# Kernel tuning notes

Measured on AMD Instinct MI355X. Metric: run time of the kernel, lower is better.

The kernel has to match this reference:

```python
import jax, jax.numpy as jnp
import numpy as np
import math

B, S, D, H, DF, L = 8, 1024, 1024, 16, 4096, 2
DK = D // H

def cosine_pe(seq_len, d_model):
    pos = jnp.arange(seq_len, dtype=jnp.float32)[:, None]
    div = jnp.exp(jnp.arange(0, d_model, 2, dtype=jnp.float32) * (-math.log(10000.0) / d_model))
    ang = pos * div[None, :]  # [S, D/2]
    # interleave sin (even cols) and cos (odd cols)
    return jnp.stack([jnp.sin(ang), jnp.cos(ang)], axis=-1).reshape(seq_len, d_model)

def layernorm(x, g, b, eps=1e-5):
    m = jnp.mean(x, axis=-1, keepdims=True)
    v = jnp.mean((x - m) ** 2, axis=-1, keepdims=True)
    return (x - m) / jnp.sqrt(v + eps) * g + b

def setup_inputs() -> dict:
    key = jax.random.key(0)
    ks = jax.random.split(key, 8)
    w = 0.03  # ~xavier scale for d_model=1024
    return {
        "q_embed_data": jax.random.normal(ks[0], (B, S, D), dtype=jnp.float32),
        "qa_embed_data": jax.random.normal(ks[1], (B, S, D), dtype=jnp.float32),
        "Wk": jax.random.normal(ks[2], (L, D, D), dtype=jnp.float32) * w,
        "bk": jnp.zeros((L, D), jnp.float32),
        "Wv": jax.random.normal(ks[3], (L, D, D), dtype=jnp.float32) * w,
        "bv": jnp.zeros((L, D), jnp.float32),
        "Wo": jax.random.normal(ks[4], (L, D, D), dtype=jnp.float32) * w,
        "bo": jnp.zeros((L, D), jnp.float32),
        "ln1_g": jnp.ones((L, D), jnp.float32),
        "ln1_b": jnp.zeros((L, D), jnp.float32),
        "W1": jax.random.normal(ks[5], (L, DF, D), dtype=jnp.float32) * w,
        "b1": jnp.zeros((L, DF), jnp.float32),
        "W2": jax.random.normal(ks[6], (L, D, DF), dtype=jnp.float32) * w,
        "b2": jnp.zeros((L, D), jnp.float32),
        "ln2_g": jnp.ones((L, D), jnp.float32),
        "ln2_b": jnp.zeros((L, D), jnp.float32),
    }

def reference(q_embed_data, qa_embed_data, Wk, bk, Wv, bv, Wo, bo, ln1_g, ln1_b, W1, b1, W2, b2, ln2_g, ln2_b):
    b, s, d = q_embed_data.shape
    pe = cosine_pe(s, d)
    x = q_embed_data + pe[None]   # query/key stream, updated per block
    y = qa_embed_data + pe[None]  # value stream, fixed across blocks
    idx = jnp.arange(s)
    allow = idx[None, :] < idx[:, None]  # strict causal: only past (j < i)
    n_blocks = Wk.shape[0]
    for l in range(n_blocks):
        # kq_same=True: q and k share k_linear
        q = (x @ Wk[l].T + bk[l]).reshape(b, s, H, DK).transpose(0, 2, 1, 3)
        k = q  # same input and same projection
        v = (y @ Wv[l].T + bv[l]).reshape(b, s, H, DK).transpose(0, 2, 1, 3)
        scores = jnp.einsum('bhid,bhjd->bhij', q, k) / math.sqrt(DK)
        scores = jnp.where(allow[None, None], scores, jnp.float32(-1e32))
        p = jax.nn.softmax(scores, axis=-1)
        p = p.at[:, :, 0, :].set(0.0)  # zero_pad first query row
        attn = jnp.einsum('bhij,bhjd->bhid', p, v).transpose(0, 2, 1, 3).reshape(b, s, d)
        attn = attn @ Wo[l].T + bo[l]
        x = layernorm(x + attn, ln1_g[l], ln1_b[l])
        ff = jax.nn.relu(x @ W1[l].T + b1[l]) @ W2[l].T + b2[l]
        x = layernorm(x + ff, ln2_g[l], ln2_b[l])
    return x
```

## Files before the change

kernel.cpp:

```cpp
#include <hip/hip_runtime.h>

using bf16   = __bf16;
using bf16x4 = __attribute__((ext_vector_type(4))) __bf16;
using bf16x8 = __attribute__((ext_vector_type(8))) __bf16;
using f32x4  = __attribute__((ext_vector_type(4))) float;

#define GLDS16(g, l)                                                            \
  __builtin_amdgcn_global_load_lds(                                             \
      (__attribute__((address_space(1))) void*)(g),                             \
      (__attribute__((address_space(3))) void*)(l), 16, 0, 0)

#define MFMA16(a, b, c) __builtin_amdgcn_mfma_f32_16x16x32_bf16(a, b, c, 0, 0, 0)

__device__ __forceinline__ int SW(int r, int s) {
  return r * 64 + (((s ^ (r & 7) ^ ((r >> 3) & 7)) & 7) << 3);
}

__device__ __forceinline__ float b2f(unsigned short u) {
  return (float)__builtin_bit_cast(bf16, u);
}

__device__ __forceinline__ bf16x8 scale8th(bf16x8 v) {
  bf16x8 r;
#pragma unroll
  for (int i = 0; i < 8; ++i) r[i] = (bf16)((float)v[i] * 0.125f);
  return r;
}

__global__ __launch_bounds__(256)
void init_pe(const float4* __restrict__ qd, const float4* __restrict__ qa,
             ushort4* __restrict__ xbf, ushort4* __restrict__ ybf) {
  const int n4 = 8 * 1024 * 1024 / 4;
  for (int i = blockIdx.x * 256 + threadIdx.x; i < n4; i += gridDim.x * 256) {
    int d4 = (i & 255) * 4;
    int ss = (i >> 8) & 1023;
    const float c = -0.0089944730195177f;
    float a0 = (float)ss * __expf((float)d4 * c);
    float a1 = (float)ss * __expf((float)(d4 + 2) * c);
    float p0 = sinf(a0), p1 = cosf(a0), p2 = sinf(a1), p3 = cosf(a1);
    float4 q4 = qd[i], y4 = qa[i];
    ushort4 xb, yb;
    xb.x = __builtin_bit_cast(unsigned short, (bf16)(q4.x + p0));
    xb.y = __builtin_bit_cast(unsigned short, (bf16)(q4.y + p1));
    xb.z = __builtin_bit_cast(unsigned short, (bf16)(q4.z + p2));
    xb.w = __builtin_bit_cast(unsigned short, (bf16)(q4.w + p3));
    yb.x = __builtin_bit_cast(unsigned short, (bf16)(y4.x + p0));
    yb.y = __builtin_bit_cast(unsigned short, (bf16)(y4.y + p1));
    yb.z = __builtin_bit_cast(unsigned short, (bf16)(y4.z + p2));
    yb.w = __builtin_bit_cast(unsigned short, (bf16)(y4.w + p3));
    xbf[i] = xb; ybf[i] = yb;
  }
}

__global__ __launch_bounds__(256)
void cvt5(const float4* __restrict__ s0, const float4* __restrict__ s1,
          const float4* __restrict__ s2, const float4* __restrict__ s3,
          const float4* __restrict__ s4,
          ushort4* __restrict__ dDD, ushort4* __restrict__ dDF,
          int n4dd, int n4df) {
  const int z = blockIdx.z;
  const float4* s = (z == 0) ? s0 : (z == 1) ? s1 : (z == 2) ? s2 : (z == 3) ? s3 : s4;
  ushort4* dd = (z < 3) ? dDD + (size_t)z * n4dd : dDF + (size_t)(z - 3) * n4df;
  const int n4 = (z < 3) ? n4dd : n4df;
  for (int i = blockIdx.x * 256 + threadIdx.x; i < n4; i += gridDim.x * 256) {
    float4 v = s[i];
    ushort4 o;
    o.x = __builtin_bit_cast(unsigned short, (bf16)v.x);
    o.y = __builtin_bit_cast(unsigned short, (bf16)v.y);
    o.z = __builtin_bit_cast(unsigned short, (bf16)v.z);
    o.w = __builtin_bit_cast(unsigned short, (bf16)v.w);
    dd[i] = o;
  }
}

template <int EPI, int MODE>
__global__ __launch_bounds__(256, 4)
void gemm_s(const bf16* __restrict__ A0, const bf16* __restrict__ W0,
            const float* __restrict__ b0, void* __restrict__ C0,
            const bf16* __restrict__ A1, const bf16* __restrict__ W1,
            const float* __restrict__ b1, void* __restrict__ C1,
            const int N, const int K) {
  __shared__ bf16 L[2][128 * 64];

  const int tid = threadIdx.x;
  const int wave = tid >> 6, lane = tid & 63;
  const int wm = wave >> 1, wn = wave & 1;
  const int cl = lane & 15, hk = lane >> 4;

  const int gx = gridDim.x;
  int flat = blockIdx.y * gx + blockIdx.x;
  flat = (flat & 7) * ((gx * gridDim.y) >> 3) + (flat >> 3);
  const int bcol = flat % gx, brow = flat / gx;
  const int z = (MODE == 0) ? 0 : blockIdx.z;

  const bf16* A = (MODE == 1 && z) ? A1 : A0;
  const bf16* W = (MODE == 1 && z) ? W1 : W0;
  const float* bias = (MODE == 1 && z) ? b1 : b0;
  void* C = (MODE == 1 && z) ? C1 : C0;

  const bf16* Ablk = A + (size_t)brow * 128 * K;
  const bf16* Wblk = W + (size_t)bcol * 128 * K;

  const int strow8 = lane >> 3;
  const int sl8 = (lane & 7) ^ (lane >> 3);

#define STAGE(kt)                                                               \
  do {                                                                          \
    _Pragma("unroll") for (int i_ = 0; i_ < 4; ++i_) {                          \
      int r0_ = i_ * 32 + wave * 8;                                             \
      GLDS16(Ablk + (size_t)(r0_ + strow8) * K + (size_t)(kt) * 64 + sl8 * 8,   \
             &L[0][r0_ * 64]);                                                  \
      GLDS16(Wblk + (size_t)(r0_ + strow8) * K + (size_t)(kt) * 64 + sl8 * 8,   \
             &L[1][r0_ * 64]);                                                  \
    }                                                                           \
  } while (0)

#define RD(reg, r_, kk_) \
  (*(const bf16x8*)&L[reg][(r_) * 64 + ((((kk_) * 4 + hk) ^ (cl & 7)) * 8)])

  f32x4 acc[4][4] = {};
  const int NT = K >> 6;

  for (int t = 0; t < NT; ++t) {
    STAGE(t);
    __syncthreads();
#pragma unroll
    for (int kk = 0; kk < 2; ++kk) {
      bf16x8 a4[4], b4[4];
#pragma unroll
      for (int m = 0; m < 4; ++m) a4[m] = RD(0, wm * 64 + m * 16 + cl, kk);
#pragma unroll
      for (int n = 0; n < 4; ++n) b4[n] = RD(1, wn * 64 + n * 16 + cl, kk);
      __builtin_amdgcn_s_setprio(1);
#pragma unroll
      for (int m = 0; m < 4; ++m)
#pragma unroll
        for (int n = 0; n < 4; ++n)
          acc[m][n] = MFMA16(a4[m], b4[n], acc[m][n]);
      __builtin_amdgcn_s_setprio(0);
    }
    __syncthreads();
  }
#undef STAGE
#undef RD

  float bv[4];
#pragma unroll
  for (int n = 0; n < 4; ++n)
    bv[n] = bias[bcol * 128 + wn * 64 + n * 16 + cl];

  const int crow0 = brow * 128 + wm * 64;
  const int ccol0 = bcol * 128 + wn * 64;
  char* esmem = (char*)(&L[0][0]) + wave * 4608;

  if (MODE == 1 && z == 1) {
    bf16* ep = (bf16*)esmem;
    const int h_ = ccol0 >> 6;
#pragma unroll
    for (int mp = 0; mp < 2; ++mp) {
#pragma unroll
      for (int mb = 0; mb < 2; ++mb) {
        int m = mp * 2 + mb;
#pragma unroll
        for (int n = 0; n < 4; ++n) {
          bf16x4 w4;
#pragma unroll
          for (int j = 0; j < 4; ++j) w4[j] = (bf16)(acc[m][n][j] + bv[n]);
          *(bf16x4*)&ep[(n * 16 + cl) * 36 + mb * 16 + hk * 4] = w4;
        }
      }
      asm volatile("s_waitcnt lgkmcnt(0)" ::: "memory");
      __builtin_amdgcn_sched_barrier(0);
      {
        const int t0 = crow0 + mp * 32;
        const int b_ = t0 >> 10, s_ = t0 & 1023;
        bf16* dst = (bf16*)C + ((size_t)(b_ * 16 + h_) * 64 + lane) * 1024 + s_;
        const bf16* src = &ep[lane * 36];
#pragma unroll
        for (int i = 0; i < 4; ++i)
          *(bf16x8*)&dst[i * 8] = *(const bf16x8*)&src[i * 8];
      }
      asm volatile("s_waitcnt lgkmcnt(0)" ::: "memory");
      __builtin_amdgcn_sched_barrier(0);
    }
  } else {
#pragma unroll
    for (int m = 0; m < 4; ++m) {
      bf16* ep = (bf16*)esmem;
#pragma unroll
      for (int n = 0; n < 4; ++n)
#pragma unroll
        for (int j = 0; j < 4; ++j) {
          float val = acc[m][n][j] + bv[n];
          if (EPI == 1) val = fmaxf(val, 0.f);
          ep[(hk * 4 + j) * 64 + n * 16 + cl] = (bf16)val;
        }
      asm volatile("s_waitcnt lgkmcnt(0)" ::: "memory");
      __builtin_amdgcn_sched_barrier(0);
#pragma unroll
      for (int i = 0; i < 2; ++i) {
        bf16x8 vv = ((const bf16x8*)ep)[lane + i * 64];
        const int row = crow0 + m * 16 + 8 * i + (lane >> 3);
        *(bf16x8*)((bf16*)C + (size_t)row * N + ccol0 + (lane & 7) * 8) = vv;
      }
      asm volatile("s_waitcnt lgkmcnt(0)" ::: "memory");
      __builtin_amdgcn_sched_barrier(0);
    }
  }
}

#define SOFTMAX_PV(sc_, diag_, mreg, lreg, oacc)                                 \
  do {                                                                           \
    if (diag_) {                                                                 \
      _Pragma("unroll") for (int c = 0; c < 4; ++c)                              \
        _Pragma("unroll") for (int j = 0; j < 4; ++j)                            \
          if (c * 16 + hk * 4 + j >= wave * 16 + cl) sc_[c][j] = -1e30f;         \
    }                                                                            \
    float rl_[4];                                                                \
    _Pragma("unroll") for (int c = 0; c < 4; ++c)                                \
      rl_[c] = fmaxf(fmaxf(sc_[c][0], sc_[c][1]), fmaxf(sc_[c][2], sc_[c][3]));  \
    float rloc_ = fmaxf(fmaxf(rl_[0], rl_[1]), fmaxf(rl_[2], rl_[3]));           \
    if (!__all(rloc_ <= mreg)) {                                                 \
      float rmx_ = fmaxf(rloc_, __shfl_xor(rloc_, 16));                          \
      rmx_ = fmaxf(rmx_, __shfl_xor(rmx_, 32));                                  \
      float mn_ = fmaxf(mreg, rmx_);                                             \
      float sca_ = __expf(mreg - mn_);                                           \
      mreg = mn_;                                                                \
      lreg *= sca_;                                                              \
      float scr_[4];                                                             \
      _Pragma("unroll") for (int j = 0; j < 4; ++j)                              \
        scr_[j] = __shfl(sca_, hk * 4 + j);                                      \
      _Pragma("unroll") for (int c = 0; c < 4; ++c)                              \
        _Pragma("unroll") for (int j = 0; j < 4; ++j) oacc[c][j] *= scr_[j];     \
    }                                                                            \
    float ps_ = 0.f;                                                             \
    if (diag_) {                                                                 \
      _Pragma("unroll") for (int c = 0; c < 4; ++c) {                            \
        bf16x4 pk_;                                                              \
        _Pragma("unroll") for (int j = 0; j < 4; ++j) {                          \
          float e_ = (sc_[c][j] < -1e29f) ? 0.f : __expf(sc_[c][j] - mreg);      \
          ps_ += e_;                                                             \
          pk_[j] = (bf16)e_;                                                     \
        }                                                                        \
        *(bf16x4*)&Pw[SW(cl, c * 2 + (hk >> 1)) + (hk & 1) * 4] = pk_;           \
      }                                                                          \
    } else {                                                                     \
      _Pragma("unroll") for (int c = 0; c < 4; ++c) {                            \
        bf16x4 pk_;                                                              \
        _Pragma("unroll") for (int j = 0; j < 4; ++j) {                          \
          float e_ = __expf(sc_[c][j] - mreg);                                   \
          ps_ += e_;                                                             \
          pk_[j] = (bf16)e_;                                                     \
        }                                                                        \
        *(bf16x4*)&Pw[SW(cl, c * 2 + (hk >> 1)) + (hk & 1) * 4] = pk_;           \
      }                                                                          \
    }                                                                            \
    lreg += ps_;                  \
    const bf16x8 pa0_ = *(const bf16x8*)&Pw[SW(cl, hk)];                         \
    const bf16x8 pa1_ = *(const bf16x8*)&Pw[SW(cl, 4 + hk)];                     \
    __builtin_amdgcn_s_setprio(1);                                               \
    _Pragma("unroll") for (int c = 0; c < 4; ++c) {                              \
      const bf16x8 vf0_ = *(const bf16x8*)&Vb[SW(c * 16 + cl, hk)];              \
      const bf16x8 vf1_ = *(const bf16x8*)&Vb[SW(c * 16 + cl, 4 + hk)];          \
      oacc[c] = MFMA16(pa0_, vf0_, oacc[c]);                                     \
      oacc[c] = MFMA16(pa1_, vf1_, oacc[c]);                                     \
    }                                                                            \
    __builtin_amdgcn_s_setprio(0);                                               \
  } while (0)

__global__ __launch_bounds__(256, 2)
void attn_kernel(const bf16* __restrict__ q, const bf16* __restrict__ vT,
                 bf16* __restrict__ out) {
  const int S = 1024, D = 1024;
  const int f = blockIdx.y * 8 + blockIdx.x;
  const int g = f >> 3, xcd = f & 7;
  const int qa = g >> 4;
  const int bh = xcd * 16 + (g & 15);
  const int qb = 15 - qa;
  const int b = bh >> 4, h = bh & 15;
  const int tid = threadIdx.x, wave = tid >> 6, lane = tid & 63;

  __shared__ bf16 Ks[2][4096];
  __shared__ bf16 Vt[2][4096];
  __shared__ bf16 Ps[4][1024];

  const bf16* qp = q + (size_t)b * S * D + h * 64;
  const bf16* vp = vT + (size_t)(b * 16 + h) * 64 * 1024;

  const int cl = lane & 15;
  const int hk = lane >> 4;
  const int r0 = hk * 4;
  const int k8 = hk * 8;

  const int ksrow = lane >> 3;
  const int ksslot = (lane & 7) ^ (lane >> 3);

  const int rA = qa * 64 + wave * 16 + cl;
  const int rB = qb * 64 + wave * 16 + cl;
  const bf16x8 qA0 = scale8th(*(const bf16x8*)(qp + (size_t)rA * D + k8));
  const bf16x8 qA1 = scale8th(*(const bf16x8*)(qp + (size_t)rA * D + 32 + k8));
  const bf16x8 qB0 = scale8th(*(const bf16x8*)(qp + (size_t)rB * D + k8));
  const bf16x8 qB1 = scale8th(*(const bf16x8*)(qp + (size_t)rB * D + 32 + k8));

  f32x4 oA[4] = {}, oB[4] = {};
  float mA_ = -1e30f, lA_ = 0.f, mB_ = -1e30f, lB_ = 0.f;

  bf16* Pw = Ps[wave];
  int buf = 0;

#define STAGE_KV(dst_ks, dst_vt, jt_)                                            \
  do {                                                                           \
    _Pragma("unroll") for (int j = 0; j < 2; ++j) {                              \
      int ch = wave * 2 + j;                                                     \
      GLDS16(qp + (size_t)((jt_) * 64 + ch * 8 + ksrow) * D +                    \
                 ((ksslot ^ (ch & 7)) * 8),                                      \
             (dst_ks) + ch * 512);                                               \
      GLDS16(vp + (size_t)(ch * 8 + ksrow) * 1024 + (jt_) * 64 +                 \
                 ((ksslot ^ (ch & 7)) * 8),                                      \
             (dst_vt) + ch * 512);                                               \
    }                                                                            \
  } while (0)

  STAGE_KV(&Ks[0][0], &Vt[0][0], 0);
  __syncthreads();

  for (int jt = 0; jt <= qb; ++jt) {
    const int nxt = buf ^ 1;
    if (jt < qb) STAGE_KV(&Ks[nxt][0], &Vt[nxt][0], jt + 1);

    {
      const bf16* Kb = Ks[buf];
      const bf16* Vb = Vt[buf];
      const bool doA = (jt <= qa);
      const bool diagB = (jt == qb), diagA = (jt == qa);

      f32x4 scB[4], scA[4];
      __builtin_amdgcn_s_setprio(1);
#pragma unroll
      for (int c = 0; c < 4; ++c) {
        int r_ = c * 16 + cl;
        const bf16x8 kf0 = *(const bf16x8*)&Kb[SW(r_, hk)];
        const bf16x8 kf1 = *(const bf16x8*)&Kb[SW(r_, 4 + hk)];
        f32x4 zB = {};
        zB = MFMA16(kf0, qB0, zB);
        zB = MFMA16(kf1, qB1, zB);
        scB[c] = zB;
        if (doA) {
          f32x4 zA = {};
          zA = MFMA16(kf0, qA0, zA);
          zA = MFMA16(kf1, qA1, zA);
          scA[c] = zA;
        }
      }
      __builtin_amdgcn_s_setprio(0);

      SOFTMAX_PV(scB, diagB, mB_, lB_, oB);
      if (doA) SOFTMAX_PV(scA, diagA, mA_, lA_, oA);
    }
    __syncthreads();
    buf = nxt;
  }
#undef STAGE_KV

  lA_ += __shfl_xor(lA_, 16);
  lA_ += __shfl_xor(lA_, 32);
  lB_ += __shfl_xor(lB_, 16);
  lB_ += __shfl_xor(lB_, 32);

  bf16* ob = out + (size_t)b * S * D + h * 64;
  const float invA = (lA_ > 0.f) ? 1.f / lA_ : 0.f;
  const float invB = (lB_ > 0.f) ? 1.f / lB_ : 0.f;
#pragma unroll
  for (int j = 0; j < 4; ++j) {
    const float iA = __shfl(invA, hk * 4 + j);
    const float iB = __shfl(invB, hk * 4 + j);
    {
      int row = qa * 64 + wave * 16 + r0 + j;
#pragma unroll
      for (int c = 0; c < 4; ++c)
        ob[(size_t)row * D + c * 16 + cl] = (bf16)(oA[c][j] * iA);
    }
    {
      int row = qb * 64 + wave * 16 + r0 + j;
#pragma unroll
      for (int c = 0; c < 4; ++c)
        ob[(size_t)row * D + c * 16 + cl] = (bf16)(oB[c][j] * iB);
    }
  }
}

__global__ __launch_bounds__(256)
void add_ln(const ushort4* __restrict__ xin, const ushort4* __restrict__ y1b,
            const float* __restrict__ g, const float* __restrict__ bt,
            ushort4* __restrict__ xbf, float4* __restrict__ xout) {
  const int row = blockIdx.x;
  const int tid = threadIdx.x;
  const int wave = tid >> 6, lane = tid & 63;
  const size_t base4 = (size_t)row * 256 + tid;
  ushort4 a4 = xin[base4];
  ushort4 c4 = y1b[base4];
  float v0 = b2f(a4.x) + b2f(c4.x), v1 = b2f(a4.y) + b2f(c4.y);
  float v2 = b2f(a4.z) + b2f(c4.z), v3 = b2f(a4.w) + b2f(c4.w);

  float s = v0 + v1 + v2 + v3;
#pragma unroll
  for (int off = 32; off; off >>= 1) s += __shfl_xor(s, off);
  __shared__ float red1[4], red2[4];
  if (lane == 0) red1[wave] = s;
  __syncthreads();
  float mean = (red1[0] + red1[1] + red1[2] + red1[3]) * (1.f / 1024.f);

  float d0 = v0 - mean, d1 = v1 - mean, d2 = v2 - mean, d3 = v3 - mean;
  float vs = d0 * d0 + d1 * d1 + d2 * d2 + d3 * d3;
#pragma unroll
  for (int off = 32; off; off >>= 1) vs += __shfl_xor(vs, off);
  if (lane == 0) red2[wave] = vs;
  __syncthreads();
  float var = (red2[0] + red2[1] + red2[2] + red2[3]) * (1.f / 1024.f);
  float rstd = rsqrtf(var + 1e-5f);

  const int col = tid * 4;
  float4 gg = *(const float4*)(g + col);
  float4 bb = *(const float4*)(bt + col);
  float o0 = d0 * rstd * gg.x + bb.x;
  float o1 = d1 * rstd * gg.y + bb.y;
  float o2 = d2 * rstd * gg.z + bb.z;
  float o3 = d3 * rstd * gg.w + bb.w;
  if (xout) {
    float4 oo; oo.x = o0; oo.y = o1; oo.z = o2; oo.w = o3;
    xout[base4] = oo;
  } else {
    ushort4 ob;
    ob.x = __builtin_bit_cast(unsigned short, (bf16)o0);
    ob.y = __builtin_bit_cast(unsigned short, (bf16)o1);
    ob.z = __builtin_bit_cast(unsigned short, (bf16)o2);
    ob.w = __builtin_bit_cast(unsigned short, (bf16)o3);
    xbf[base4] = ob;
  }
}

extern "C" void kernel_launch(void* const* d_in, const int* in_sizes, int n_in,
                              void* d_out, int out_size, void* d_ws, size_t ws_size,
                              hipStream_t stream) {
  const float* qd  = (const float*)d_in[0];
  const float* qa  = (const float*)d_in[1];
  const float* Wk  = (const float*)d_in[2];
  const float* bk  = (const float*)d_in[3];
  const float* Wv  = (const float*)d_in[4];
  const float* bv  = (const float*)d_in[5];
  const float* Wo  = (const float*)d_in[6];
  const float* bo  = (const float*)d_in[7];
  const float* l1g = (const float*)d_in[8];
  const float* l1b = (const float*)d_in[9];
  const float* W1  = (const float*)d_in[10];
  const float* b1  = (const float*)d_in[11];
  const float* W2  = (const float*)d_in[12];
  const float* b2  = (const float*)d_in[13];
  const float* l2g = (const float*)d_in[14];
  const float* l2b = (const float*)d_in[15];

  const size_t DD = 1024 * 1024, DFD = 4096 * 1024, T = 8192;
  bf16* wkb = (bf16*)d_ws;
  bf16* wvb = wkb + 2 * DD;
  bf16* wob = wvb + 2 * DD;
  bf16* w1b = wob + 2 * DD;
  bf16* w2b = w1b + 2 * DFD;
  bf16* regA = w2b + 2 * DFD;
  bf16* qbf = regA;
  bf16* vbf = regA + 8388608;
  bf16* abf = regA + 16777216;
  bf16* ff1 = regA;
  bf16* xbf = regA + 33554432;
  bf16* ybf = xbf + 8388608;
  bf16* g1b = ybf + 8388608;

  init_pe<<<2048, 256, 0, stream>>>((const float4*)qd, (const float4*)qa,
                                    (ushort4*)xbf, (ushort4*)ybf);
  cvt5<<<dim3(1024, 1, 5), 256, 0, stream>>>(
      (const float4*)Wk, (const float4*)Wv, (const float4*)Wo,
      (const float4*)W1, (const float4*)W2,
      (ushort4*)wkb, (ushort4*)w1b, (int)(2 * DD / 4), (int)(2 * DFD / 4));

  for (int l = 0; l < 2; ++l) {
    gemm_s<0, 1><<<dim3(8, 64, 2), 256, 0, stream>>>(
        xbf, wkb + l * DD, bk + l * 1024, qbf,
        ybf, wvb + l * DD, bv + l * 1024, vbf, 1024, 1024);
    attn_kernel<<<dim3(8, 128), 256, 0, stream>>>(qbf, vbf, abf);
    gemm_s<0, 0><<<dim3(8, 64), 256, 0, stream>>>(
        abf, wob + l * DD, bo + l * 1024, g1b, nullptr, nullptr, nullptr, nullptr, 1024, 1024);
    add_ln<<<T, 256, 0, stream>>>((const ushort4*)xbf, (const ushort4*)g1b,
                                  l1g + l * 1024, l1b + l * 1024,
                                  (ushort4*)xbf, nullptr);
    gemm_s<1, 0><<<dim3(32, 64), 256, 0, stream>>>(
        xbf, w1b + l * DFD, b1 + l * 4096, ff1, nullptr, nullptr, nullptr, nullptr, 4096, 1024);
    gemm_s<0, 0><<<dim3(8, 64), 256, 0, stream>>>(
        ff1, w2b + l * DFD, b2 + l * 1024, g1b, nullptr, nullptr, nullptr, nullptr, 1024, 4096);
    const bool last = (l == 1);
    add_ln<<<T, 256, 0, stream>>>((const ushort4*)xbf, (const ushort4*)g1b,
                                  l2g + l * 1024, l2b + l * 1024,
                                  (ushort4*)xbf, last ? (float4*)d_out : nullptr);
  }
  (void)in_sizes; (void)n_in; (void)out_size; (void)ws_size;
}
```

Measured before the change: 614.9 us.

## Add 256x256-tile 8-wave pipelined GEMM for the FFN up-projection

Adds a new GEMM kernel with 256x256 output tiles, 512 threads (8 waves), double-buffered LDS staged via global_load_lds, and a four-phase interleaved load/MFMA schedule with setprio and an XCD-aware block remap. It replaces the previous 128-wide gemm_s for the W1 + ReLU projection. The intent is more data reuse per LDS load and better overlap of global loads with MFMA work on the largest GEMM. The cost is 128KB of dynamic LDS, which limits occupancy, and fewer blocks (512) for the GPU to spread across its CUs.

```diff
diff --git a/kernel.cpp b/kernel.cpp
--- a/kernel.cpp
+++ b/kernel.cpp
@@ -207,6 +207,180 @@
       __builtin_amdgcn_sched_barrier(0);
     }
   }
+}
+
+template <int EPI>
+__global__ __launch_bounds__(512, 2)
+void gemm8(const bf16* __restrict__ A, const bf16* __restrict__ W,
+           const float* __restrict__ bias, bf16* __restrict__ C,
+           const int N, const int K) {
+  extern __shared__ bf16 lds[];
+
+  const int tid = threadIdx.x;
+  const int wave = tid >> 6, lane = tid & 63;
+  const int wm = wave >> 2, wn = wave & 3;
+  const int cl = lane & 15, hk = lane >> 4;
+  const int sl8 = (lane & 7) ^ (lane >> 3);
+
+  const int gx = gridDim.x;
+  int flat = blockIdx.y * gx + blockIdx.x;
+  flat = (flat & 7) * ((gx * gridDim.y) >> 3) + (flat >> 3);
+  const int bcol = flat % gx, brow = flat / gx;
+
+  const bf16* Ablk = A + (size_t)brow * 256 * K;
+  const bf16* Wblk = W + (size_t)bcol * 256 * K;
+  const size_t srow = (size_t)(wave * 8 + (lane >> 3)) * K + sl8 * 8;
+
+  const int NT = K >> 6;
+
+#define STG8(src, r0, dstbase, kt)                                             \
+  do {                                                                         \
+    _Pragma("unroll") for (int i_ = 0; i_ < 2; ++i_)                           \
+      GLDS16((src) + srow + (size_t)((r0) + i_ * 64) * K + (size_t)(kt) * 64,  \
+             (dstbase) + ((r0) + i_ * 64 + wave * 8) * 64);                    \
+  } while (0)
+
+#define RDF(base, r, kk) \
+  (*(const bf16x8*)&(base)[(r) * 64 + ((((kk) * 4 + hk) ^ ((r) & 7)) * 8)])
+
+#define BAR8 asm volatile("s_barrier" ::: "memory")
+
+  STG8(Ablk, 0, lds, 0);
+  STG8(Ablk, 128, lds, 0);
+  STG8(Wblk, 0, lds + 16384, 0);
+  STG8(Wblk, 128, lds + 16384, 0);
+  STG8(Wblk, 0, lds + 49152, 1);
+  STG8(Ablk, 0, lds + 32768, 1);
+  asm volatile("s_waitcnt vmcnt(4)" ::: "memory");
+  BAR8;
+
+  f32x4 acc[2][2][4][2] = {};
+  bf16x8 a[2][4], b0[2][2], b1[2][2];
+
+  for (int t = 0; t < NT; ++t) {
+    bf16* Ab = lds + (t & 1) * 32768;
+    bf16* Bb = Ab + 16384;
+    bf16* An = lds + (((t & 1) ^ 1)) * 32768;
+    bf16* Bn = An + 16384;
+
+#pragma unroll
+    for (int kk = 0; kk < 2; ++kk) {
+#pragma unroll
+      for (int m_ = 0; m_ < 4; ++m_)
+        a[kk][m_] = RDF(Ab, wm * 128 + m_ * 16 + cl, kk);
+#pragma unroll
+      for (int n_ = 0; n_ < 2; ++n_)
+        b0[kk][n_] = RDF(Bb, wn * 64 + n_ * 16 + cl, kk);
+    }
+    if (t + 1 < NT) STG8(Ablk, 128, An, t + 1);
+    BAR8;
+    __builtin_amdgcn_s_setprio(1);
+#pragma unroll
+    for (int kk = 0; kk < 2; ++kk)
+#pragma unroll
+      for (int m_ = 0; m_ < 4; ++m_)
+#pragma unroll
+        for (int n_ = 0; n_ < 2; ++n_)
+          acc[0][0][m_][n_] = MFMA16(a[kk][m_], b0[kk][n_], acc[0][0][m_][n_]);
+    __builtin_amdgcn_s_setprio(0);
+    BAR8;
+
+#pragma unroll
+    for (int kk = 0; kk < 2; ++kk)
+#pragma unroll
+      for (int n_ = 0; n_ < 2; ++n_)
+        b1[kk][n_] = RDF(Bb, wn * 64 + 32 + n_ * 16 + cl, kk);
+    if (t + 1 < NT) STG8(Wblk, 128, Bn, t + 1);
+    BAR8;
+    __builtin_amdgcn_s_setprio(1);
+#pragma unroll
+    for (int kk = 0; kk < 2; ++kk)
+#pragma unroll
+      for (int m_ = 0; m_ < 4; ++m_)
+#pragma unroll
+        for (int n_ = 0; n_ < 2; ++n_)
+          acc[0][1][m_][n_] = MFMA16(a[kk][m_], b1[kk][n_], acc[0][1][m_][n_]);
+    __builtin_amdgcn_s_setprio(0);
+    BAR8;
+
+#pragma unroll
+    for (int kk = 0; kk < 2; ++kk)
+#pragma unroll
+      for (int m_ = 0; m_ < 4; ++m_)
+        a[kk][m_] = RDF(Ab, wm * 128 + 64 + m_ * 16 + cl, kk);
+    if (t + 2 < NT) STG8(Wblk, 0, Bb, t + 2);
+    BAR8;
+    __builtin_amdgcn_s_setprio(1);
+#pragma unroll
+    for (int kk = 0; kk < 2; ++kk)
+#pragma unroll
+      for (int m_ = 0; m_ < 4; ++m_)
+#pragma unroll
+        for (int n_ = 0; n_ < 2; ++n_)
+          acc[1][0][m_][n_] = MFMA16(a[kk][m_], b0[kk][n_], acc[1][0][m_][n_]);
+    __builtin_amdgcn_s_setprio(0);
+    BAR8;
+
+    if (t + 2 < NT) {
+      STG8(Ablk, 0, Ab, t + 2);
+      asm volatile("s_waitcnt vmcnt(4)" ::: "memory");
+    } else if (t + 1 < NT) {
+      asm volatile("s_waitcnt vmcnt(0)" ::: "memory");
+    }
+    BAR8;
+    __builtin_amdgcn_s_setprio(1);
+#pragma unroll
+    for (int kk = 0; kk < 2; ++kk)
+#pragma unroll
+      for (int m_ = 0; m_ < 4; ++m_)
+#pragma unroll
+        for (int n_ = 0; n_ < 2; ++n_)
+          acc[1][1][m_][n_] = MFMA16(a[kk][m_], b1[kk][n_], acc[1][1][m_][n_]);
+    __builtin_amdgcn_s_setprio(0);
+    BAR8;
+  }
+#undef STG8
+#undef RDF
+#undef BAR8
+
+  __syncthreads();
+
+  float bv[2][2];
+#pragma unroll
+  for (int nh = 0; nh < 2; ++nh)
+#pragma unroll
+    for (int n_ = 0; n_ < 2; ++n_)
+      bv[nh][n_] = bias[bcol * 256 + wn * 64 + nh * 32 + n_ * 16 + cl];
+
+  const int crow0 = brow * 256 + wm * 128;
+  const int ccol0 = bcol * 256 + wn * 64;
+  bf16* ep = lds + wave * 2304;
+
+#pragma unroll
+  for (int mh = 0; mh < 2; ++mh)
+#pragma unroll
+    for (int m_ = 0; m_ < 4; ++m_) {
+#pragma unroll
+      for (int nh = 0; nh < 2; ++nh)
+#pragma unroll
+        for (int n_ = 0; n_ < 2; ++n_)
+#pragma unroll
+          for (int j = 0; j < 4; ++j) {
+            float val = acc[mh][nh][m_][n_][j] + bv[nh][n_];
+            if (EPI == 1) val = fmaxf(val, 0.f);
+            ep[(hk * 4 + j) * 64 + nh * 32 + n_ * 16 + cl] = (bf16)val;
+          }
+      asm volatile("s_waitcnt lgkmcnt(0)" ::: "memory");
+      __builtin_amdgcn_sched_barrier(0);
+#pragma unroll
+      for (int i = 0; i < 2; ++i) {
+        bf16x8 vv = ((const bf16x8*)ep)[lane + i * 64];
+        const int row = crow0 + mh * 64 + m_ * 16 + 8 * i + (lane >> 3);
+        *(bf16x8*)(C + (size_t)row * N + ccol0 + (lane & 7) * 8) = vv;
+      }
+      asm volatile("s_waitcnt lgkmcnt(0)" ::: "memory");
+      __builtin_amdgcn_sched_barrier(0);
+    }
 }
 
 #define SOFTMAX_PV(sc_, diag_, mreg, lreg, oacc)                                 \
@@ -474,6 +648,13 @@
   bf16* ybf = xbf + 8388608;
   bf16* g1b = ybf + 8388608;
 
+  static bool gemm8_attr = false;
+  if (!gemm8_attr) {
+    (void)hipFuncSetAttribute(reinterpret_cast<const void*>(&gemm8<1>),
+                              hipFuncAttributeMaxDynamicSharedMemorySize, 131072);
+    gemm8_attr = true;
+  }
+
   init_pe<<<2048, 256, 0, stream>>>((const float4*)qd, (const float4*)qa,
                                     (ushort4*)xbf, (ushort4*)ybf);
   cvt5<<<dim3(1024, 1, 5), 256, 0, stream>>>(
@@ -491,8 +672,8 @@
     add_ln<<<T, 256, 0, stream>>>((const ushort4*)xbf, (const ushort4*)g1b,
                                   l1g + l * 1024, l1b + l * 1024,
                                   (ushort4*)xbf, nullptr);
-    gemm_s<1, 0><<<dim3(32, 64), 256, 0, stream>>>(
-        xbf, w1b + l * DFD, b1 + l * 4096, ff1, nullptr, nullptr, nullptr, nullptr, 4096, 1024);
+    gemm8<1><<<dim3(16, 32), 512, 131072, stream>>>(
+        xbf, w1b + l * DFD, b1 + l * 4096, ff1, 4096, 1024);
     gemm_s<0, 0><<<dim3(8, 64), 256, 0, stream>>>(
         ff1, w2b + l * DFD, b2 + l * 1024, g1b, nullptr, nullptr, nullptr, nullptr, 1024, 4096);
     const bool last = (l == 1);
```

Measured after the change: 612.8 us. Within noise of the previous version (-0.3%).
